# Optimization experiments

Hardware: AMD Instinct MI355X
Metric: run time of the kernel (lower is better)

The kernel has to match this reference:

```python
import jax, jax.numpy as jnp
import numpy as np

EPS = 1e-8  # torch.nn.CosineSimilarity eps


def setup_inputs() -> dict:
    key = jax.random.key(0)
    k1, k2, k3 = jax.random.split(key, 3)
    C, S, D = 1024, 16, 512
    x = jax.random.normal(k1, (C, S, D), dtype=jnp.float32)
    w = jax.random.normal(k2, (1,), dtype=jnp.float32)
    b = jax.random.normal(k3, (1,), dtype=jnp.float32)
    return {"x": x, "w": w, "b": b}


def reference(x, w, b):
    # stable_ge2e: leave-one-out positive centroids, full negative centroids.
    C, S, D = x.shape
    wp = jax.nn.softplus(w)  # (1,)

    sum_c = x.sum(axis=1)                      # (C, D)
    mean_c = sum_c / S                         # negative centroids (C, D)
    loo = (sum_c[:, None, :] - x) / (S - 1.0)  # leave-one-out centroids (C, S, D)

    nx = jnp.linalg.norm(x, axis=-1)           # (C, S)
    nmean = jnp.linalg.norm(mean_c, axis=-1)   # (C,)
    nloo = jnp.linalg.norm(loo, axis=-1)       # (C, S)

    # cosine similarities (clamped denominator, as in torch CosineSimilarity)
    sim_neg = jnp.einsum('jid,kd->jik', x, mean_c) / jnp.maximum(
        nx[:, :, None] * nmean[None, None, :], EPS)          # (C, S, C)
    sim_pos = jnp.einsum('jid,jid->ji', x, loo) / jnp.maximum(nx * nloo, EPS)  # (C, S)

    # on the diagonal k == j use the leave-one-out positive centroid
    eye = jnp.eye(C, dtype=bool)
    sim = jnp.where(eye[:, None, :], sim_pos[:, :, None], sim_neg)  # (C, S, C)

    logits = wp * sim + b
    logS = jax.nn.log_softmax(logits, axis=-1)
    Sji_j = jnp.einsum('jij->ji', logS)                        # (C, S) diagonal
    Sji_k = jax.scipy.special.logsumexp(logS, axis=-1)         # (C, S) (== 0 post-softmax)
    loss = -(Sji_j - Sji_k).reshape(-1)
    return loss.mean()
```

## Files before the change

### kernel.cpp

```cpp
#include <hip/hip_runtime.h>
#include <math.h>

#define CC 1024
#define SS 16
#define DD 512
#define RR (CC*SS)
#define EPSV 1e-8f
#define LDB 520

typedef __attribute__((ext_vector_type(8))) short short8;
typedef __attribute__((ext_vector_type(4))) float f32x4;
typedef unsigned short ushort_t;

__device__ __forceinline__ unsigned short f2bf(float f) {
  unsigned u = __float_as_uint(f);
  u += 0x7fffu + ((u >> 16) & 1u);
  return (unsigned short)(u >> 16);
}

__device__ __forceinline__ void async16(void* l, const void* g) {
  __builtin_amdgcn_global_load_lds(
      (const __attribute__((address_space(1))) void*)g,
      (__attribute__((address_space(3))) void*)l, 16, 0, 0);
}

__device__ __forceinline__ float softplusf(float v) {
  return (v > 20.f) ? v : log1pf(expf(v));
}

__global__ __launch_bounds__(256) void k_pre(
    const float* __restrict__ x, ushort_t* __restrict__ mn,
    float* __restrict__ nx, float* __restrict__ simpos,
    ushort_t* __restrict__ xn) {
  __shared__ float xs[SS * DD];
  __shared__ float sums[DD];
  __shared__ float red[4];
  __shared__ float snm;
  __shared__ float rinv[SS];
  const int j = blockIdx.x, tid = threadIdx.x;
  const float4* xj = (const float4*)(x + (size_t)j * SS * DD);
  float4* xs4 = (float4*)xs;
  for (int i = tid; i < SS * DD / 4; i += 256) xs4[i] = xj[i];
  __syncthreads();
  float m2 = 0.f;
  for (int d = tid; d < DD; d += 256) {
    float s = 0.f;
#pragma unroll
    for (int i = 0; i < SS; ++i) s += xs[i * DD + d];
    sums[d] = s;
    float m = s * (1.0f / SS);
    m2 += m * m;
  }
#pragma unroll
  for (int off = 32; off > 0; off >>= 1) m2 += __shfl_xor(m2, off, 64);
  const int wid = tid >> 6, lane = tid & 63;
  if (lane == 0) red[wid] = m2;
  __syncthreads();
  if (tid == 0) snm = sqrtf(red[0] + red[1] + red[2] + red[3]);
  __syncthreads();
  const float inm = (1.0f / SS) / snm;
  for (int d = tid; d < DD; d += 256)
    mn[(size_t)j * DD + d] = f2bf(sums[d] * inm);
  for (int i = wid; i < SS; i += 4) {
    float nx2 = 0.f, dxs = 0.f, t2 = 0.f;
    for (int d = lane; d < DD; d += 64) {
      float xv = xs[i * DD + d];
      float sc = sums[d];
      nx2 = fmaf(xv, xv, nx2);
      dxs = fmaf(xv, sc, dxs);
      float tv = sc - xv;
      t2 = fmaf(tv, tv, t2);
    }
#pragma unroll
    for (int off = 32; off > 0; off >>= 1) {
      nx2 += __shfl_xor(nx2, off, 64);
      dxs += __shfl_xor(dxs, off, 64);
      t2  += __shfl_xor(t2,  off, 64);
    }
    if (lane == 0) {
      float nxv = sqrtf(nx2);
      float tn  = sqrtf(t2);
      float num = (dxs - nx2) * (1.0f / (SS - 1));
      float den = fmaxf(nxv * tn * (1.0f / (SS - 1)), EPSV);
      nx[j * SS + i] = nxv;
      rinv[i] = 1.0f / nxv;
      simpos[j * SS + i] = num / den;
    }
  }
  __syncthreads();
  if (xn) {
    unsigned* dst = (unsigned*)(xn + (size_t)j * SS * DD);
    for (int idx = tid; idx < SS * DD / 2; idx += 256) {
      const int e = idx * 2;
      const float ri = rinv[e >> 9];
      unsigned lo = f2bf(xs[e] * ri);
      unsigned hi = f2bf(xs[e + 1] * ri);
      dst[idx] = lo | (hi << 16);
    }
  }
}

template <bool USE_XN>
__global__ __launch_bounds__(256) void k_gemm(
    const float* __restrict__ x, const ushort_t* __restrict__ xn,
    const ushort_t* __restrict__ mn, const float* __restrict__ nx,
    const float* __restrict__ simpos, const float* __restrict__ wptr,
    const float* __restrict__ bptr, float* __restrict__ ps) {
  __shared__ ushort_t bs[2][64 * LDB];
  const int tid = threadIdx.x;
  const int wid = tid >> 6, lane = tid & 63;
  const int cL = lane & 15, quad = lane >> 4;
  const int rb = (int)blockIdx.x >> 1, cb = (int)blockIdx.x & 1;
  const int r0 = rb * 128, cbase = cb * 512;
  const float wp = softplusf(wptr[0]), bv = bptr[0];

  short8 af[2][16];
  int jw[2];
  float sp[2][4], sacc[2][4];
#pragma unroll
  for (int rt = 0; rt < 2; ++rt) {
    const int row = r0 + wid * 32 + rt * 16 + cL;
    if (USE_XN) {
      const short8* src = (const short8*)(xn + (size_t)row * DD);
#pragma unroll
      for (int kc = 0; kc < 16; ++kc) af[rt][kc] = src[kc * 4 + quad];
    } else {
      const float* xr = x + (size_t)row * DD;
      const float invn = 1.0f / nx[row];
#pragma unroll
      for (int kc = 0; kc < 16; ++kc) {
        const int k0 = kc * 32 + quad * 8;
        float4 p = *(const float4*)(xr + k0);
        float4 q = *(const float4*)(xr + k0 + 4);
        short8 v;
        v[0] = f2bf(p.x * invn); v[1] = f2bf(p.y * invn);
        v[2] = f2bf(p.z * invn); v[3] = f2bf(p.w * invn);
        v[4] = f2bf(q.x * invn); v[5] = f2bf(q.y * invn);
        v[6] = f2bf(q.z * invn); v[7] = f2bf(q.w * invn);
        af[rt][kc] = v;
      }
    }
    jw[rt] = (r0 + wid * 32 + rt * 16) >> 4;
#pragma unroll
    for (int r = 0; r < 4; ++r) {
      sp[rt][r] = simpos[r0 + wid * 32 + rt * 16 + quad * 4 + r];
      sacc[rt][r] = 0.f;
    }
  }

  {
    const ushort_t* gsrc = mn + (size_t)cbase * DD;
#pragma unroll
    for (int t = 0; t < 16; ++t) {
      const int rr = wid + t * 4;
      async16(&bs[0][rr * LDB + lane * 8], gsrc + (size_t)rr * DD + lane * 8);
    }
  }
  __syncthreads();

  for (int cc = 0; cc < 8; ++cc) {
    if (cc < 7) {
      const ushort_t* gsrc = mn + (size_t)(cbase + (cc + 1) * 64) * DD;
      ushort_t* dst = bs[(cc + 1) & 1];
#pragma unroll
      for (int t = 0; t < 16; ++t) {
        const int rr = wid + t * 4;
        async16(&dst[rr * LDB + lane * 8], gsrc + (size_t)rr * DD + lane * 8);
      }
    }
    const ushort_t* B = bs[cc & 1];
    f32x4 acc[2][4];
#pragma unroll
    for (int rt = 0; rt < 2; ++rt)
#pragma unroll
      for (int f = 0; f < 4; ++f) acc[rt][f] = (f32x4){0.f, 0.f, 0.f, 0.f};
#pragma unroll
    for (int kc = 0; kc < 16; ++kc) {
      short8 bfr[4];
#pragma unroll
      for (int f = 0; f < 4; ++f)
        bfr[f] = *(const short8*)&B[(f * 16 + cL) * LDB + kc * 32 + quad * 8];
#pragma unroll
      for (int rt = 0; rt < 2; ++rt)
#pragma unroll
        for (int f = 0; f < 4; ++f)
          acc[rt][f] = __builtin_amdgcn_mfma_f32_16x16x32_bf16(
              af[rt][kc], bfr[f], acc[rt][f], 0, 0, 0);
    }
    const int c0 = cbase + cc * 64;
#pragma unroll
    for (int rt = 0; rt < 2; ++rt)
#pragma unroll
      for (int f = 0; f < 4; ++f) {
        const int cg = c0 + f * 16 + cL;
        const bool diag = (cg == jw[rt]);
#pragma unroll
        for (int r = 0; r < 4; ++r) {
          const float sim = diag ? sp[rt][r] : acc[rt][f][r];
          sacc[rt][r] += __expf(fmaf(wp, sim, bv));
        }
      }
    __syncthreads();
  }

#pragma unroll
  for (int rt = 0; rt < 2; ++rt)
#pragma unroll
    for (int r = 0; r < 4; ++r) {
      float v = sacc[rt][r];
#pragma unroll
      for (int off = 1; off < 16; off <<= 1) v += __shfl_xor(v, off, 64);
      if (cL == 0)
        ps[(size_t)(r0 + wid * 32 + rt * 16 + quad * 4 + r) * 2 + cb] = v;
    }
}

__global__ __launch_bounds__(256) void k_combine(
    const float* __restrict__ ps, const float* __restrict__ simpos,
    const float* __restrict__ wptr, const float* __restrict__ bptr,
    float* __restrict__ p2) {
  __shared__ float red[4];
  const int tid = threadIdx.x;
  const int row = blockIdx.x * 256 + tid;
  const float wp = softplusf(wptr[0]), bv = bptr[0];
  const float s = ps[row * 2] + ps[row * 2 + 1];
  float v = logf(s) - fmaf(wp, simpos[row], bv);
#pragma unroll
  for (int off = 32; off > 0; off >>= 1) v += __shfl_xor(v, off, 64);
  if ((tid & 63) == 0) red[tid >> 6] = v;
  __syncthreads();
  if (tid == 0) p2[blockIdx.x] = red[0] + red[1] + red[2] + red[3];
}

__global__ __launch_bounds__(64) void k_fin(const float* __restrict__ p2,
                                            float* __restrict__ out) {
  const int tid = threadIdx.x;
  float v = p2[tid];
#pragma unroll
  for (int off = 32; off > 0; off >>= 1) v += __shfl_xor(v, off, 64);
  if (tid == 0) out[0] = v * (1.0f / RR);
}

extern "C" void kernel_launch(void* const* d_in, const int* in_sizes, int n_in,
                              void* d_out, int out_size, void* d_ws, size_t ws_size,
                              hipStream_t stream) {
  const float* x = (const float*)d_in[0];
  const float* w = (const float*)d_in[1];
  const float* b = (const float*)d_in[2];
  float* out = (float*)d_out;

  const size_t xn_bytes = (size_t)RR * DD * 2;
  const size_t rest = (size_t)CC * DD * 2 + (size_t)RR * 4 * 2 +
                      (size_t)RR * 2 * 4 + 64 * 4;
  const bool use_xn = ws_size >= xn_bytes + rest + 256;

  char* base = (char*)d_ws;
  ushort_t* xn = use_xn ? (ushort_t*)base : nullptr;
  char* p = base + (use_xn ? xn_bytes : 0);
  ushort_t* mn = (ushort_t*)p;  p += (size_t)CC * DD * 2;
  float* nx     = (float*)p;    p += (size_t)RR * 4;
  float* simpos = (float*)p;    p += (size_t)RR * 4;
  float* ps     = (float*)p;    p += (size_t)RR * 2 * 4;
  float* p2     = (float*)p;

  k_pre<<<CC, 256, 0, stream>>>(x, mn, nx, simpos, xn);
  if (use_xn)
    k_gemm<true><<<256, 256, 0, stream>>>(x, xn, mn, nx, simpos, w, b, ps);
  else
    k_gemm<false><<<256, 256, 0, stream>>>(x, xn, mn, nx, simpos, w, b, ps);
  k_combine<<<RR / 256, 256, 0, stream>>>(ps, simpos, w, b, p2);
  k_fin<<<1, 64, 0, stream>>>(p2, out);
}
```

Baseline: 114.6 us.

## Split GEMM columns four ways and widen stores in preprocessing kernel

```diff
diff --git a/kernel.cpp b/kernel.cpp
--- a/kernel.cpp
+++ b/kernel.cpp
@@ -29,7 +29,7 @@
 }
 
 __global__ __launch_bounds__(256) void k_pre(
-    const float* __restrict__ x, ushort_t* __restrict__ mn,
+    const float* __restrict__ x, unsigned* __restrict__ mn,
     float* __restrict__ nx, float* __restrict__ simpos,
     ushort_t* __restrict__ xn) {
   __shared__ float xs[SS * DD];
@@ -43,13 +43,17 @@
   for (int i = tid; i < SS * DD / 4; i += 256) xs4[i] = xj[i];
   __syncthreads();
   float m2 = 0.f;
-  for (int d = tid; d < DD; d += 256) {
-    float s = 0.f;
-#pragma unroll
-    for (int i = 0; i < SS; ++i) s += xs[i * DD + d];
-    sums[d] = s;
-    float m = s * (1.0f / SS);
-    m2 += m * m;
+  {
+    const int d0 = tid * 2;
+    float s0 = 0.f, s1 = 0.f;
+#pragma unroll
+    for (int i = 0; i < SS; ++i) {
+      s0 += xs[i * DD + d0];
+      s1 += xs[i * DD + d0 + 1];
+    }
+    sums[d0] = s0; sums[d0 + 1] = s1;
+    float ma = s0 * (1.0f / SS), mb = s1 * (1.0f / SS);
+    m2 = fmaf(ma, ma, mb * mb);
   }
 #pragma unroll
   for (int off = 32; off > 0; off >>= 1) m2 += __shfl_xor(m2, off, 64);
@@ -59,8 +63,12 @@
   if (tid == 0) snm = sqrtf(red[0] + red[1] + red[2] + red[3]);
   __syncthreads();
   const float inm = (1.0f / SS) / snm;
-  for (int d = tid; d < DD; d += 256)
-    mn[(size_t)j * DD + d] = f2bf(sums[d] * inm);
+  {
+    const int d0 = tid * 2;
+    unsigned lo = f2bf(sums[d0] * inm);
+    unsigned hi = f2bf(sums[d0 + 1] * inm);
+    mn[((size_t)j * DD + d0) >> 1] = lo | (hi << 16);
+  }
   for (int i = wid; i < SS; i += 4) {
     float nx2 = 0.f, dxs = 0.f, t2 = 0.f;
     for (int d = lane; d < DD; d += 64) {
@@ -89,29 +97,29 @@
   }
   __syncthreads();
   if (xn) {
-    unsigned* dst = (unsigned*)(xn + (size_t)j * SS * DD);
-    for (int idx = tid; idx < SS * DD / 2; idx += 256) {
-      const int e = idx * 2;
+    uint2* dst = (uint2*)(xn + (size_t)j * SS * DD);
+    for (int idx = tid; idx < SS * DD / 4; idx += 256) {
+      const int e = idx * 4;
       const float ri = rinv[e >> 9];
-      unsigned lo = f2bf(xs[e] * ri);
-      unsigned hi = f2bf(xs[e + 1] * ri);
-      dst[idx] = lo | (hi << 16);
+      unsigned a = f2bf(xs[e] * ri),     b2 = f2bf(xs[e + 1] * ri);
+      unsigned c = f2bf(xs[e + 2] * ri), d2 = f2bf(xs[e + 3] * ri);
+      dst[idx] = make_uint2(a | (b2 << 16), c | (d2 << 16));
     }
   }
 }
 
 template <bool USE_XN>
-__global__ __launch_bounds__(256) void k_gemm(
+__global__ __launch_bounds__(256, 2) void k_gemm(
     const float* __restrict__ x, const ushort_t* __restrict__ xn,
     const ushort_t* __restrict__ mn, const float* __restrict__ nx,
     const float* __restrict__ simpos, const float* __restrict__ wptr,
     const float* __restrict__ bptr, float* __restrict__ ps) {
-  __shared__ ushort_t bs[2][64 * LDB];
+  __shared__ ushort_t bs[2][32 * LDB];
   const int tid = threadIdx.x;
   const int wid = tid >> 6, lane = tid & 63;
   const int cL = lane & 15, quad = lane >> 4;
-  const int rb = (int)blockIdx.x >> 1, cb = (int)blockIdx.x & 1;
-  const int r0 = rb * 128, cbase = cb * 512;
+  const int rb = (int)blockIdx.x >> 2, cb = (int)blockIdx.x & 3;
+  const int r0 = rb * 128, cbase = cb * 256;
   const float wp = softplusf(wptr[0]), bv = bptr[0];
 
   short8 af[2][16];
@@ -151,7 +159,7 @@
   {
     const ushort_t* gsrc = mn + (size_t)cbase * DD;
 #pragma unroll
-    for (int t = 0; t < 16; ++t) {
+    for (int t = 0; t < 8; ++t) {
       const int rr = wid + t * 4;
       async16(&bs[0][rr * LDB + lane * 8], gsrc + (size_t)rr * DD + lane * 8);
     }
@@ -160,38 +168,38 @@
 
   for (int cc = 0; cc < 8; ++cc) {
     if (cc < 7) {
-      const ushort_t* gsrc = mn + (size_t)(cbase + (cc + 1) * 64) * DD;
+      const ushort_t* gsrc = mn + (size_t)(cbase + (cc + 1) * 32) * DD;
       ushort_t* dst = bs[(cc + 1) & 1];
 #pragma unroll
-      for (int t = 0; t < 16; ++t) {
+      for (int t = 0; t < 8; ++t) {
         const int rr = wid + t * 4;
         async16(&dst[rr * LDB + lane * 8], gsrc + (size_t)rr * DD + lane * 8);
       }
     }
     const ushort_t* B = bs[cc & 1];
-    f32x4 acc[2][4];
+    f32x4 acc[2][2];
 #pragma unroll
     for (int rt = 0; rt < 2; ++rt)
 #pragma unroll
-      for (int f = 0; f < 4; ++f) acc[rt][f] = (f32x4){0.f, 0.f, 0.f, 0.f};
+      for (int f = 0; f < 2; ++f) acc[rt][f] = (f32x4){0.f, 0.f, 0.f, 0.f};
 #pragma unroll
     for (int kc = 0; kc < 16; ++kc) {
-      short8 bfr[4];
-#pragma unroll
-      for (int f = 0; f < 4; ++f)
+      short8 bfr[2];
+#pragma unroll
+      for (int f = 0; f < 2; ++f)
         bfr[f] = *(const short8*)&B[(f * 16 + cL) * LDB + kc * 32 + quad * 8];
 #pragma unroll
       for (int rt = 0; rt < 2; ++rt)
 #pragma unroll
-        for (int f = 0; f < 4; ++f)
+        for (int f = 0; f < 2; ++f)
           acc[rt][f] = __builtin_amdgcn_mfma_f32_16x16x32_bf16(
               af[rt][kc], bfr[f], acc[rt][f], 0, 0, 0);
     }
-    const int c0 = cbase + cc * 64;
+    const int c0 = cbase + cc * 32;
 #pragma unroll
     for (int rt = 0; rt < 2; ++rt)
 #pragma unroll
-      for (int f = 0; f < 4; ++f) {
+      for (int f = 0; f < 2; ++f) {
         const int cg = c0 + f * 16 + cL;
         const bool diag = (cg == jw[rt]);
 #pragma unroll
@@ -211,7 +219,7 @@
 #pragma unroll
       for (int off = 1; off < 16; off <<= 1) v += __shfl_xor(v, off, 64);
       if (cL == 0)
-        ps[(size_t)(r0 + wid * 32 + rt * 16 + quad * 4 + r) * 2 + cb] = v;
+        ps[(size_t)(r0 + wid * 32 + rt * 16 + quad * 4 + r) * 4 + cb] = v;
     }
 }
 
@@ -223,7 +231,8 @@
   const int tid = threadIdx.x;
   const int row = blockIdx.x * 256 + tid;
   const float wp = softplusf(wptr[0]), bv = bptr[0];
-  const float s = ps[row * 2] + ps[row * 2 + 1];
+  const float4 s4 = *(const float4*)(ps + (size_t)row * 4);
+  const float s = (s4.x + s4.y) + (s4.z + s4.w);
   float v = logf(s) - fmaf(wp, simpos[row], bv);
 #pragma unroll
   for (int off = 32; off > 0; off >>= 1) v += __shfl_xor(v, off, 64);
@@ -251,7 +260,7 @@
 
   const size_t xn_bytes = (size_t)RR * DD * 2;
   const size_t rest = (size_t)CC * DD * 2 + (size_t)RR * 4 * 2 +
-                      (size_t)RR * 2 * 4 + 64 * 4;
+                      (size_t)RR * 4 * 4 + 64 * 4;
   const bool use_xn = ws_size >= xn_bytes + rest + 256;
 
   char* base = (char*)d_ws;
@@ -260,14 +269,14 @@
   ushort_t* mn = (ushort_t*)p;  p += (size_t)CC * DD * 2;
   float* nx     = (float*)p;    p += (size_t)RR * 4;
   float* simpos = (float*)p;    p += (size_t)RR * 4;
-  float* ps     = (float*)p;    p += (size_t)RR * 2 * 4;
+  float* ps     = (float*)p;    p += (size_t)RR * 4 * 4;
   float* p2     = (float*)p;
 
-  k_pre<<<CC, 256, 0, stream>>>(x, mn, nx, simpos, xn);
+  k_pre<<<CC, 256, 0, stream>>>(x, (unsigned*)mn, nx, simpos, xn);
   if (use_xn)
-    k_gemm<true><<<256, 256, 0, stream>>>(x, xn, mn, nx, simpos, w, b, ps);
+    k_gemm<true><<<512, 256, 0, stream>>>(x, xn, mn, nx, simpos, w, b, ps);
   else
-    k_gemm<false><<<256, 256, 0, stream>>>(x, xn, mn, nx, simpos, w, b, ps);
+    k_gemm<false><<<512, 256, 0, stream>>>(x, xn, mn, nx, simpos, w, b, ps);
   k_combine<<<RR / 256, 256, 0, stream>>>(ps, simpos, w, b, p2);
   k_fin<<<1, 64, 0, stream>>>(p2, out);
 }
```

Measured after the change: 115.0 us. No clear change (+0.3%).
